# Optimization experiments

Hardware: AMD Instinct MI355X
Metric: run time of the kernel (lower is better)

## Reference

```python
import jax, jax.numpy as jnp
import numpy as np

D_G = 16384; B = 128; NNZ = 262144
CL1_F = 32; CL1_K = 6; FC1_F = 512; FC2_F = 512
NN_FC1 = 512; NN_FC2 = 256
CL4_F = 32; CL4_K = 4; FC1_G4 = 128; FC2_G4 = 64
OUT = 10; POOL1 = 8; POOL4 = 3; V4 = 10; EMB = 64
FC1FIN = CL1_F * (D_G // POOL1)        # 65536
G4OUT = CL4_F * (OUT // POOL4)         # 96
SUMFIN = FC1_F + NN_FC2 + FC2_G4 + 64  # 896


def _cheby(x, W, b, spmm, K):
    # x: [B, V, Fin]; Chebyshev recursion T_k(L) x with K-order feature stacking
    Bb, V, Fin = x.shape
    x0 = jnp.transpose(x, (1, 2, 0)).reshape(V, Fin * Bb)
    xs = [x0]
    if K > 1:
        x1 = spmm(x0)
        xs.append(x1)
        for _ in range(K - 2):
            x2 = 2.0 * spmm(x1) - x0
            xs.append(x2)
            x0, x1 = x1, x2
    X = jnp.stack(xs).reshape(K, V, Fin, Bb)
    X = jnp.transpose(X, (3, 1, 2, 0)).reshape(Bb * V, Fin * K)  # [B*V, Fin*K]
    return (X @ W.T + b).reshape(Bb, V, -1)


def _gmaxpool(x, p):
    # MaxPool1d(p) over node dim (floor truncation like torch)
    Bb, V, F = x.shape
    Vp = (V // p) * p
    return x[:, :Vp].reshape(Bb, V // p, p, F).max(axis=2)


def setup_inputs():
    key = jax.random.key(0)
    ks = jax.random.split(key, 32)
    def lin(i, fo, fi):
        return (jax.random.normal(ks[i], (fo, fi), jnp.float32) * 0.02,
                jnp.zeros((fo,), jnp.float32))
    cl1_W, cl1_b = lin(0, CL1_F, CL1_K)
    fc1_W, fc1_b = lin(1, FC1_F, FC1FIN)
    fc2_W, fc2_b = lin(2, FC2_F, FC1_F)
    fc3_W, fc3_b = lin(3, D_G, FC2_F)
    nn1_W, nn1_b = lin(4, NN_FC1, D_G)
    nn2_W, nn2_b = lin(5, NN_FC2, NN_FC1)
    cl4_W, cl4_b = lin(6, CL4_F, CL4_K * EMB)
    fcg1_W, fcg1_b = lin(7, FC1_G4, G4OUT)
    fcg2_W, fcg2_b = lin(8, FC2_G4, FC1_G4)
    nn14_W, nn14_b = lin(9, 256, V4 * EMB)
    nn24_W, nn24_b = lin(10, 64, 256)
    fcsum_W, fcsum_b = lin(11, OUT, SUMFIN)
    return {
        'x_in': jax.random.normal(ks[12], (B, D_G), jnp.float32),
        'x_embed': jax.random.normal(ks[13], (V4, EMB), jnp.float32),
        'dropout': 0,
        'L_rows': jnp.sort(jax.random.randint(ks[14], (NNZ,), 0, D_G)),
        'L_cols': jax.random.randint(ks[15], (NNZ,), 0, D_G),
        'L_vals': jax.random.normal(ks[16], (NNZ,), jnp.float32) * 0.1,
        'L_mg': jax.random.normal(ks[17], (V4, V4), jnp.float32) * 0.2,
        'cl1_W': cl1_W, 'cl1_b': cl1_b, 'fc1_W': fc1_W, 'fc1_b': fc1_b,
        'fc2_W': fc2_W, 'fc2_b': fc2_b, 'fc3_W': fc3_W, 'fc3_b': fc3_b,
        'nn1_W': nn1_W, 'nn1_b': nn1_b, 'nn2_W': nn2_W, 'nn2_b': nn2_b,
        'cl4_W': cl4_W, 'cl4_b': cl4_b, 'fcg1_W': fcg1_W, 'fcg1_b': fcg1_b,
        'fcg2_W': fcg2_W, 'fcg2_b': fcg2_b, 'nn14_W': nn14_W, 'nn14_b': nn14_b,
        'nn24_W': nn24_W, 'nn24_b': nn24_b, 'fcsum_W': fcsum_W, 'fcsum_b': fcsum_b,
    }


def reference(x_in, x_embed, dropout, L_rows, L_cols, L_vals, L_mg,
              cl1_W, cl1_b, fc1_W, fc1_b, fc2_W, fc2_b, fc3_W, fc3_b,
              nn1_W, nn1_b, nn2_W, nn2_b, cl4_W, cl4_b,
              fcg1_W, fcg1_b, fcg2_W, fcg2_b, nn14_W, nn14_b, nn24_W, nn24_b,
              fcsum_W, fcsum_b):
    Bb = x_in.shape[0]
    def spmm_L(m):  # COO SpMM: y[r] += v * m[c]
        return jax.ops.segment_sum(L_vals[:, None] * m[L_cols], L_rows,
                                   num_segments=D_G)
    # --- GCN 1 (gene graph) ---
    x = _cheby(x_in[:, :, None], cl1_W, cl1_b, spmm_L, CL1_K)
    x = jax.nn.relu(x)
    x = _gmaxpool(x, POOL1).reshape(Bb, FC1FIN)
    x_hidden_gae = jax.nn.relu(x @ fc1_W.T + fc1_b)
    # FC2_F != 0 branch; dropout p=0 is identity at this baseline
    x_decode_gae = jax.nn.relu(x_hidden_gae @ fc2_W.T + fc2_b)
    x_decode_gae = x_decode_gae @ fc3_W.T + fc3_b
    # --- NN 1 ---
    x_nn = jax.nn.relu(x_in @ nn1_W.T + nn1_b)
    x_nn = jax.nn.relu(x_nn @ nn2_W.T + nn2_b)
    # --- GCN 4 (small meta-graph, dense Laplacian) ---
    xe = jnp.broadcast_to(x_embed[None], (Bb, V4, EMB))
    xg = _cheby(xe, cl4_W, cl4_b, lambda m: L_mg @ m, CL4_K)
    xg = jax.nn.relu(xg)
    xg = _gmaxpool(xg, POOL4).reshape(Bb, G4OUT)
    xg = jax.nn.relu(xg @ fcg1_W.T + fcg1_b)
    xg = jax.nn.relu(xg @ fcg2_W.T + fcg2_b)
    # --- NN of GCN4 ---
    xn4 = xe.reshape(Bb, V4 * EMB)
    xn4 = jax.nn.relu(xn4 @ nn14_W.T + nn14_b)
    xn4 = jax.nn.relu(xn4 @ nn24_W.T + nn24_b)
    data_emb = jnp.concatenate([x_hidden_gae, x_nn, xg, xn4], axis=1)
    logp = jax.nn.log_softmax(data_emb @ fcsum_W.T + fcsum_b, axis=-1)
    return x_decode_gae, x_hidden_gae, logp
```

## Files before the change

kernel.cpp:

```cpp
#include <hip/hip_runtime.h>
#include <hip/hip_bf16.h>

#define DG 16384
#define NNZ 262144
#define BB 128

typedef __attribute__((ext_vector_type(8))) short bf16x8;
typedef __attribute__((ext_vector_type(8))) unsigned short us8;
typedef __attribute__((ext_vector_type(4))) float f32x4;
typedef __attribute__((ext_vector_type(4))) unsigned short us4;
typedef __attribute__((ext_vector_type(2))) float f32x2;

#define WS_ROWPTR 0
#define WS_XIN16  66048
#define WS_T      4260352
#define WS_XPOOL  54592000
#define WS_XB0    71369216
#define WS_XB1    75563520
#define WS_XNN1B  79757824
#define WS_DEC2   79888896
#define WS_XNN2   80019968
#define WS_HIDB   80151040
#define WS_N1     80282112
#define WS_TAIL   80283136
#define WS_PNN1   81000448
#define WS_PFC1   97777664

__device__ __forceinline__ unsigned short f2bf(float f) {
  __hip_bfloat16 h = __float2bfloat16(f);
  return __builtin_bit_cast(unsigned short, h);
}
__device__ __forceinline__ float bflo(unsigned u) {
  return __builtin_bit_cast(float, u << 16);
}
__device__ __forceinline__ float bfhi(unsigned u) {
  return __builtin_bit_cast(float, u & 0xffff0000u);
}
__device__ __forceinline__ f32x4 ntload4(const float* p) {
  return __builtin_nontemporal_load((const f32x4*)p);
}

__device__ void prep_dev(const float* __restrict__ x_in, const int* __restrict__ rows,
                         int* __restrict__ rowptr, unsigned short* __restrict__ xin16,
                         int bid) {
  int idx = bid * 256 + threadIdx.x;
  if (idx <= DG) {
    int lo = 0, hi = NNZ;
    while (lo < hi) { int mid = (lo + hi) >> 1; if (rows[mid] < idx) lo = mid + 1; else hi = mid; }
    rowptr[idx] = lo;
  }
  f32x4 v = ((const f32x4*)x_in)[idx];
  us4 o; o[0] = f2bf(v[0]); o[1] = f2bf(v[1]); o[2] = f2bf(v[2]); o[3] = f2bf(v[3]);
  ((us4*)xin16)[idx] = o;
}

__device__ void transpose_dev(const float* __restrict__ x_in, float* __restrict__ T0,
                              unsigned short* __restrict__ Xb0, int id) {
  __shared__ float tl[32][33];
  int bx = id & 511, by = id >> 9;
  int v0 = bx * 32, b0 = by * 32;
  int tx = threadIdx.x & 31, ty0 = threadIdx.x >> 5;
  #pragma unroll
  for (int j = 0; j < 4; ++j) {
    int ty = ty0 + j * 8;
    tl[ty][tx] = x_in[(size_t)(b0 + ty) * DG + v0 + tx];
  }
  __syncthreads();
  #pragma unroll
  for (int j = 0; j < 4; ++j) {
    int ty = ty0 + j * 8;
    float v = tl[tx][ty];
    size_t o = (size_t)(v0 + ty) * BB + b0 + tx;
    T0[o] = v;
    Xb0[o] = f2bf(v);
  }
}

__device__ void dot4_dev(const float* __restrict__ x, const float* __restrict__ W,
                         const float* __restrict__ bias, float* __restrict__ out,
                         int K, int id) {
  int w = threadIdx.x >> 6, lane = threadIdx.x & 63;
  int o = id * 4 + w;
  float a = 0.f;
  for (int i = lane; i < K; i += 64) a += x[i] * W[(size_t)o * K + i];
  #pragma unroll
  for (int s = 32; s > 0; s >>= 1) a += __shfl_down(a, s);
  if (lane == 0) out[o] = fmaxf(a + bias[o], 0.f);
}

__device__ void g4_dev(const float* __restrict__ xe_g, const float* __restrict__ Lmg_g,
                       const float* __restrict__ W4, const float* __restrict__ b4,
                       const float* __restrict__ Wg1, const float* __restrict__ bg1,
                       const float* __restrict__ Wg2, const float* __restrict__ bg2,
                       float* __restrict__ tail) {
  __shared__ float Lm[100], Tg[4][640], xc[320], xg96[96], h1[128];
  int t = threadIdx.x;
  for (int i = t; i < 640; i += 256) Tg[0][i] = xe_g[i];
  for (int i = t; i < 100; i += 256) Lm[i] = Lmg_g[i];
  __syncthreads();
  for (int i = t; i < 640; i += 256) {
    int v = i >> 6, f = i & 63; float s = 0.f;
    #pragma unroll
    for (int u = 0; u < 10; ++u) s += Lm[v * 10 + u] * Tg[0][u * 64 + f];
    Tg[1][i] = s;
  }
  __syncthreads();
  for (int kk = 2; kk < 4; ++kk) {
    for (int i = t; i < 640; i += 256) {
      int v = i >> 6, f = i & 63; float s = 0.f;
      #pragma unroll
      for (int u = 0; u < 10; ++u) s += Lm[v * 10 + u] * Tg[kk - 1][u * 64 + f];
      Tg[kk][i] = 2.f * s - Tg[kk - 2][i];
    }
    __syncthreads();
  }
  for (int i = t; i < 320; i += 256) {
    int v = i >> 5, fo = i & 31; float s = b4[fo];
    for (int fin = 0; fin < 64; ++fin)
      #pragma unroll
      for (int k = 0; k < 4; ++k) s += Tg[k][v * 64 + fin] * W4[fo * 256 + fin * 4 + k];
    xc[i] = fmaxf(s, 0.f);
  }
  __syncthreads();
  for (int i = t; i < 96; i += 256) {
    int g = i >> 5, fo = i & 31;
    xg96[i] = fmaxf(fmaxf(xc[(3 * g) * 32 + fo], xc[(3 * g + 1) * 32 + fo]),
                    xc[(3 * g + 2) * 32 + fo]);
  }
  __syncthreads();
  for (int o = t; o < 128; o += 256) {
    float s = bg1[o];
    for (int i2 = 0; i2 < 96; ++i2) s += xg96[i2] * Wg1[o * 96 + i2];
    h1[o] = fmaxf(s, 0.f);
  }
  __syncthreads();
  for (int o = t; o < 64; o += 256) {
    float s = bg2[o];
    for (int i2 = 0; i2 < 128; ++i2) s += h1[i2] * Wg2[o * 128 + i2];
    tail[o] = fmaxf(s, 0.f);
  }
}

__global__ __launch_bounds__(256) void setup_kernel(
    const float* __restrict__ x_in, const int* __restrict__ rows,
    int* __restrict__ rowptr, unsigned short* __restrict__ xin16,
    float* __restrict__ T0, unsigned short* __restrict__ Xb0,
    const float* __restrict__ x_embed,
    const float* __restrict__ nn14_W, const float* __restrict__ nn14_b,
    float* __restrict__ n1,
    const float* __restrict__ Lmg, const float* __restrict__ W4,
    const float* __restrict__ b4, const float* __restrict__ Wg1,
    const float* __restrict__ bg1, const float* __restrict__ Wg2,
    const float* __restrict__ bg2, float* __restrict__ tail) {
  int bid = blockIdx.x;
  if (bid < 1) g4_dev(x_embed, Lmg, W4, b4, Wg1, bg1, Wg2, bg2, tail);
  else if (bid < 65) dot4_dev(x_embed, nn14_W, nn14_b, n1, 640, bid - 1);
  else if (bid < 2113) prep_dev(x_in, rows, rowptr, xin16, bid - 65);
  else transpose_dev(x_in, T0, Xb0, bid - 2113);
}

__global__ __launch_bounds__(256) void spmm3(
    const int* __restrict__ rowptr, const int* __restrict__ cols,
    const float* __restrict__ vals, const unsigned* __restrict__ X2,
    const float* __restrict__ Tprev, float* __restrict__ Tout,
    unsigned* __restrict__ Xbout, float scale) {
  int r = blockIdx.x * 4 + (threadIdx.x >> 6);
  int lane = threadIdx.x & 63;
  int e0 = rowptr[r], e1 = rowptr[r + 1];
  float a00 = 0.f, a01 = 0.f, a10 = 0.f, a11 = 0.f;
  int e = e0;
  for (; e + 4 <= e1; e += 4) {
    int c0 = cols[e], c1 = cols[e + 1], c2 = cols[e + 2], c3 = cols[e + 3];
    float v0 = vals[e], v1 = vals[e + 1], v2 = vals[e + 2], v3 = vals[e + 3];
    unsigned x0 = X2[c0 * 64 + lane], x1 = X2[c1 * 64 + lane];
    unsigned x2 = X2[c2 * 64 + lane], x3 = X2[c3 * 64 + lane];
    a00 += v0 * bflo(x0); a10 += v0 * bfhi(x0);
    a01 += v1 * bflo(x1); a11 += v1 * bfhi(x1);
    a00 += v2 * bflo(x2); a10 += v2 * bfhi(x2);
    a01 += v3 * bflo(x3); a11 += v3 * bfhi(x3);
  }
  for (; e < e1; ++e) {
    float v = vals[e]; unsigned x = X2[cols[e] * 64 + lane];
    a00 += v * bflo(x); a10 += v * bfhi(x);
  }
  float s0 = scale * (a00 + a01), s1 = scale * (a10 + a11);
  size_t o = (size_t)r * BB + lane * 2;
  if (Tprev) { f32x2 p = *(const f32x2*)(Tprev + o); s0 -= p[0]; s1 -= p[1]; }
  *(f32x2*)(Tout + o) = (f32x2){s0, s1};
  Xbout[(size_t)r * 64 + lane] = (unsigned)f2bf(s0) | ((unsigned)f2bf(s1) << 16);
}

__device__ void combine_dev(const float* __restrict__ Tbase, const float* __restrict__ W,
                            const float* __restrict__ bias, unsigned short* __restrict__ xpool,
                            int vp) {
  __shared__ float tile[6][8][128];
  __shared__ float Wl[192];
  __shared__ float bl[32];
  for (int i = threadIdx.x; i < 192; i += 256) Wl[i] = W[i];
  if (threadIdx.x < 32) bl[threadIdx.x] = bias[threadIdx.x];
  for (int i = threadIdx.x; i < 6144; i += 256) {
    int k = i >> 10, rem = i & 1023, j = rem >> 7, b = rem & 127;
    tile[k][j][b] = Tbase[(size_t)k * 2097152 + (size_t)(vp * 8 + j) * BB + b];
  }
  __syncthreads();
  for (int p = threadIdx.x; p < 4096; p += 256) {
    int b = p >> 5, f = p & 31;
    float m = -1e30f;
    #pragma unroll
    for (int j = 0; j < 8; ++j) {
      float s = bl[f];
      #pragma unroll
      for (int k = 0; k < 6; ++k) s += tile[k][j][b] * Wl[f * 6 + k];
      m = fmaxf(m, s);
    }
    m = fmaxf(m, 0.f);
    xpool[(size_t)b * 65536 + vp * 32 + f] = f2bf(m);
  }
}

__global__ __launch_bounds__(256) void combine_nn24(
    const float* __restrict__ Tbase, const float* __restrict__ W,
    const float* __restrict__ bias, unsigned short* __restrict__ xpool,
    const float* __restrict__ n1, const float* __restrict__ nn24_W,
    const float* __restrict__ nn24_b, float* __restrict__ tail64) {
  int bid = blockIdx.x;
  if (bid < 2048) combine_dev(Tbase, W, bias, xpool, bid);
  else dot4_dev(n1, nn24_W, nn24_b, tail64, 256, bid - 2048);
}

template<int NT, int MT>
__device__ void gemm_core5(
    unsigned short* __restrict__ Alds,
    const unsigned short* __restrict__ A, const float* __restrict__ W,
    float* __restrict__ outP, unsigned short* __restrict__ outB,
    const float* __restrict__ bias, int K, int N, int Kchunk,
    int bx, int by, int row0, int relu, int partial) {
  const int LA = MT / 2;
  int t = threadIdx.x, w = t >> 6, lane = t & 63, lr = lane & 15, lg = lane >> 4;
  int n0 = bx * NT * 64;
  int kbeg = by * Kchunk;
  f32x4 acc[MT][NT];
  #pragma unroll
  for (int mt = 0; mt < MT; ++mt)
    #pragma unroll
    for (int nt = 0; nt < NT; ++nt) acc[mt][nt] = (f32x4){0.f, 0.f, 0.f, 0.f};
  const float* Wbase = W + (size_t)(n0 + w * NT * 16 + lr) * K + lg * 8;
  int stages = Kchunk >> 6;
  for (int s = 0; s < stages; ++s) {
    int k0 = kbeg + s * 64;
    f32x4 rw[NT][4];
    #pragma unroll
    for (int nt = 0; nt < NT; ++nt) {
      const float* wp = Wbase + (size_t)nt * 16 * K + k0;
      rw[nt][0] = ntload4(wp);      rw[nt][1] = ntload4(wp + 4);
      rw[nt][2] = ntload4(wp + 32); rw[nt][3] = ntload4(wp + 36);
    }
    __syncthreads();
    #pragma unroll
    for (int j = 0; j < LA; ++j) {
      int idx = j * 256 + t;
      int row = idx >> 3, kk = (idx & 7) * 8;
      us8 v = *(const us8*)(A + (size_t)(row0 + row) * K + k0 + kk);
      *(us8*)(Alds + row * 64 + (kk ^ ((row & 7) << 3))) = v;
    }
    __syncthreads();
    #pragma unroll
    for (int h = 0; h < 2; ++h) {
      int k32 = h * 32;
      bf16x8 bfr[NT];
      #pragma unroll
      for (int nt = 0; nt < NT; ++nt) {
        f32x4 w0 = rw[nt][h * 2], w1 = rw[nt][h * 2 + 1];
        bf16x8 bv;
        bv[0] = (short)f2bf(w0[0]); bv[1] = (short)f2bf(w0[1]);
        bv[2] = (short)f2bf(w0[2]); bv[3] = (short)f2bf(w0[3]);
        bv[4] = (short)f2bf(w1[0]); bv[5] = (short)f2bf(w1[1]);
        bv[6] = (short)f2bf(w1[2]); bv[7] = (short)f2bf(w1[3]);
        bfr[nt] = bv;
      }
      #pragma unroll
      for (int mt = 0; mt < MT; ++mt) {
        int arow = mt * 16 + lr;
        bf16x8 af = *(const bf16x8*)(Alds + arow * 64 + ((k32 + lg * 8) ^ ((arow & 7) << 3)));
        #pragma unroll
        for (int nt = 0; nt < NT; ++nt)
          acc[mt][nt] = __builtin_amdgcn_mfma_f32_16x16x32_bf16(af, bfr[nt], acc[mt][nt], 0, 0, 0);
      }
    }
  }
  if (partial) {
    float* P = outP + (size_t)by * 128 * (size_t)N;
    #pragma unroll
    for (int mt = 0; mt < MT; ++mt)
      #pragma unroll
      for (int nt = 0; nt < NT; ++nt) {
        int col = n0 + w * NT * 16 + nt * 16 + lr;
        #pragma unroll
        for (int r2 = 0; r2 < 4; ++r2) {
          int row = row0 + mt * 16 + lg * 4 + r2;
          P[(size_t)row * N + col] = acc[mt][nt][r2];
        }
      }
  } else {
    #pragma unroll
    for (int mt = 0; mt < MT; ++mt)
      #pragma unroll
      for (int nt = 0; nt < NT; ++nt) {
        int col = n0 + w * NT * 16 + nt * 16 + lr;
        float bc = bias[col];
        #pragma unroll
        for (int r2 = 0; r2 < 4; ++r2) {
          int row = row0 + mt * 16 + lg * 4 + r2;
          float v = acc[mt][nt][r2] + bc;
          if (relu) v = fmaxf(v, 0.f);
          if (outP) outP[(size_t)row * N + col] = v;
          if (outB) outB[(size_t)row * N + col] = f2bf(v);
        }
      }
  }
}

__global__ __launch_bounds__(256, 4) void gemm_partials(
    const unsigned short* __restrict__ xin16, const float* __restrict__ nn1_W,
    const unsigned short* __restrict__ xpool, const float* __restrict__ fc1_W,
    float* __restrict__ pnn1, float* __restrict__ pfc1) {
  __shared__ unsigned short Alds[128 * 64];
  int nb = blockIdx.x;
  if (nb < 128) {
    int xcd = nb & 7, q = nb >> 3, bx = q & 3, by = ((q >> 2) << 3) | xcd;
    gemm_core5<2, 8>(Alds, xin16, nn1_W, pnn1, nullptr, nullptr,
                     16384, 512, 512, bx, by, 0, 0, 1);
  } else {
    int b = nb - 128;
    int xcd = b & 7, q = b >> 3, bx = q & 3, by = ((q >> 2) << 3) | xcd;
    gemm_core5<2, 8>(Alds, xpool, fc1_W, pfc1, nullptr, nullptr,
                     65536, 512, 512, bx, by, 0, 0, 1);
  }
}

__global__ __launch_bounds__(256) void reduce_fused(
    const float* __restrict__ pfc1, const float* __restrict__ fc1_b,
    float* __restrict__ hidden, unsigned short* __restrict__ hidB,
    const float* __restrict__ pnn1, const float* __restrict__ nn1_b,
    unsigned short* __restrict__ xnn1b) {
  int b = blockIdx.x;
  if (b < 256) {
    int idx = b * 256 + threadIdx.x;
    float s = 0.f;
    for (int i = 0; i < 128; ++i) s += pfc1[(size_t)i * 65536 + idx];
    float v = fmaxf(s + fc1_b[idx & 511], 0.f);
    hidden[idx] = v;
    hidB[idx] = f2bf(v);
  } else {
    int idx = (b - 256) * 256 + threadIdx.x;
    float s = 0.f;
    for (int i = 0; i < 32; ++i) s += pnn1[(size_t)i * 65536 + idx];
    float v = fmaxf(s + nn1_b[idx & 511], 0.f);
    xnn1b[idx] = f2bf(v);
  }
}

__global__ __launch_bounds__(256, 4) void fc2nn2_kernel(
    const unsigned short* __restrict__ hidB, const float* __restrict__ fc2_W,
    const float* __restrict__ fc2_b, unsigned short* __restrict__ dec2,
    const unsigned short* __restrict__ xnn1b, const float* __restrict__ nn2_W,
    const float* __restrict__ nn2_b, float* __restrict__ xnn2) {
  __shared__ unsigned short Alds[128 * 64];
  int b = blockIdx.x;
  if (b < 8)
    gemm_core5<1, 8>(Alds, hidB, fc2_W, nullptr, dec2, fc2_b,
                     512, 512, 512, b, 0, 0, 1, 0);
  else
    gemm_core5<1, 8>(Alds, xnn1b, nn2_W, xnn2, nullptr, nn2_b,
                     512, 256, 512, b - 8, 0, 0, 1, 0);
}

__device__ void fcsum_dev(int id, const float* __restrict__ hidden,
                          const float* __restrict__ xnn2, const float* __restrict__ tail,
                          const float* __restrict__ Ws, const float* __restrict__ bs,
                          float* __restrict__ logp) {
  __shared__ float emb[4][896];
  int w = threadIdx.x >> 6, lane = threadIdx.x & 63;
  int b = id * 4 + w;
  for (int i = lane; i < 896; i += 64)
    emb[w][i] = (i < 512) ? hidden[b * 512 + i]
              : (i < 768) ? xnn2[b * 256 + (i - 512)]
                          : tail[i - 768];
  __syncthreads();
  float l[10];
  #pragma unroll
  for (int o = 0; o < 10; ++o) {
    float a = 0.f;
    for (int i = lane; i < 896; i += 64) a += emb[w][i] * Ws[o * 896 + i];
    #pragma unroll
    for (int s = 32; s > 0; s >>= 1) a += __shfl_down(a, s);
    l[o] = __shfl(a, 0) + bs[o];
  }
  float m = l[0];
  #pragma unroll
  for (int o = 1; o < 10; ++o) m = fmaxf(m, l[o]);
  float sum = 0.f;
  #pragma unroll
  for (int o = 0; o < 10; ++o) sum += expf(l[o] - m);
  float lse = m + logf(sum);
  #pragma unroll
  for (int o = 0; o < 10; ++o)
    if (lane == o) logp[b * 10 + o] = l[o] - lse;
}

__global__ __launch_bounds__(256, 4) void fc3_head(
    const unsigned short* __restrict__ dec2, const float* __restrict__ fc3_W,
    const float* __restrict__ fc3_b, float* __restrict__ out0,
    const float* __restrict__ hidden, const float* __restrict__ xnn2,
    const float* __restrict__ tail, const float* __restrict__ fcsum_W,
    const float* __restrict__ fcsum_b, float* __restrict__ logp) {
  __shared__ unsigned short Alds[64 * 64];
  int b = blockIdx.x;
  if (b < 512) {
    int bx = b >> 1, my = b & 1;
    gemm_core5<1, 4>(Alds, dec2, fc3_W, out0, nullptr, fc3_b,
                     512, 16384, 512, bx, 0, my * 64, 0, 0);
  } else {
    fcsum_dev(b - 512, hidden, xnn2, tail, fcsum_W, fcsum_b, logp);
  }
}

extern "C" void kernel_launch(void* const* d_in, const int* in_sizes, int n_in,
                              void* d_out, int out_size, void* d_ws, size_t ws_size,
                              hipStream_t stream) {
  const float* x_in    = (const float*)d_in[0];
  const float* x_embed = (const float*)d_in[1];
  const int*   L_rows  = (const int*)d_in[3];
  const int*   L_cols  = (const int*)d_in[4];
  const float* L_vals  = (const float*)d_in[5];
  const float* L_mg    = (const float*)d_in[6];
  const float* cl1_W = (const float*)d_in[7],  *cl1_b = (const float*)d_in[8];
  const float* fc1_W = (const float*)d_in[9],  *fc1_b = (const float*)d_in[10];
  const float* fc2_W = (const float*)d_in[11], *fc2_b = (const float*)d_in[12];
  const float* fc3_W = (const float*)d_in[13], *fc3_b = (const float*)d_in[14];
  const float* nn1_W = (const float*)d_in[15], *nn1_b = (const float*)d_in[16];
  const float* nn2_W = (const float*)d_in[17], *nn2_b = (const float*)d_in[18];
  const float* cl4_W = (const float*)d_in[19], *cl4_b = (const float*)d_in[20];
  const float* fcg1_W = (const float*)d_in[21], *fcg1_b = (const float*)d_in[22];
  const float* fcg2_W = (const float*)d_in[23], *fcg2_b = (const float*)d_in[24];
  const float* nn14_W = (const float*)d_in[25], *nn14_b = (const float*)d_in[26];
  const float* nn24_W = (const float*)d_in[27], *nn24_b = (const float*)d_in[28];
  const float* fcsum_W = (const float*)d_in[29], *fcsum_b = (const float*)d_in[30];

  char* ws = (char*)d_ws;
  int* rowptr = (int*)(ws + WS_ROWPTR);
  unsigned short* xin16 = (unsigned short*)(ws + WS_XIN16);
  float* T = (float*)(ws + WS_T);
  unsigned short* xpool = (unsigned short*)(ws + WS_XPOOL);
  unsigned short* Xb0 = (unsigned short*)(ws + WS_XB0);
  unsigned short* Xb1 = (unsigned short*)(ws + WS_XB1);
  unsigned short* xnn1b = (unsigned short*)(ws + WS_XNN1B);
  unsigned short* dec2 = (unsigned short*)(ws + WS_DEC2);
  float* xnn2 = (float*)(ws + WS_XNN2);
  unsigned short* hidB = (unsigned short*)(ws + WS_HIDB);
  float* n1 = (float*)(ws + WS_N1);
  float* tail = (float*)(ws + WS_TAIL);
  float* pnn1 = (float*)(ws + WS_PNN1);
  float* pfc1 = (float*)(ws + WS_PFC1);

  float* out0 = (float*)d_out;
  float* hidden = out0 + 2097152;
  float* logp = out0 + 2097152 + 65536;

  setup_kernel<<<4161, 256, 0, stream>>>(x_in, L_rows, rowptr, xin16, T, Xb0,
                                         x_embed, nn14_W, nn14_b, n1,
                                         L_mg, cl4_W, cl4_b, fcg1_W, fcg1_b,
                                         fcg2_W, fcg2_b, tail);

  spmm3<<<4096, 256, 0, stream>>>(rowptr, L_cols, L_vals, (const unsigned*)Xb0,
                                  nullptr,          T + 1 * 2097152, (unsigned*)Xb1, 1.f);
  spmm3<<<4096, 256, 0, stream>>>(rowptr, L_cols, L_vals, (const unsigned*)Xb1,
                                  T,                T + 2 * 2097152, (unsigned*)Xb0, 2.f);
  spmm3<<<4096, 256, 0, stream>>>(rowptr, L_cols, L_vals, (const unsigned*)Xb0,
                                  T + 1 * 2097152,  T + 3 * 2097152, (unsigned*)Xb1, 2.f);
  spmm3<<<4096, 256, 0, stream>>>(rowptr, L_cols, L_vals, (const unsigned*)Xb1,
                                  T + 2 * 2097152,  T + 4 * 2097152, (unsigned*)Xb0, 2.f);
  spmm3<<<4096, 256, 0, stream>>>(rowptr, L_cols, L_vals, (const unsigned*)Xb0,
                                  T + 3 * 2097152,  T + 5 * 2097152, (unsigned*)Xb1, 2.f);

  combine_nn24<<<2064, 256, 0, stream>>>(T, cl1_W, cl1_b, xpool,
                                         n1, nn24_W, nn24_b, tail + 64);

  gemm_partials<<<640, 256, 0, stream>>>(xin16, nn1_W, xpool, fc1_W, pnn1, pfc1);

  reduce_fused<<<512, 256, 0, stream>>>(pfc1, fc1_b, hidden, hidB,
                                        pnn1, nn1_b, xnn1b);

  fc2nn2_kernel<<<12, 256, 0, stream>>>(hidB, fc2_W, fc2_b, dec2,
                                        xnn1b, nn2_W, nn2_b, xnn2);

  fc3_head<<<544, 256, 0, stream>>>(dec2, fc3_W, fc3_b, out0,
                                    hidden, xnn2, tail, fcsum_W, fcsum_b, logp);
}
```

Baseline: 284.9 us.

## Stage converted weight tiles in LDS and use full 128-row tiles for fc2/nn2/fc3

Adds a GEMM core that loads each 64x64 fp32 weight tile once per stage, converts it to bf16 into swizzled shared memory, and has all waves read MFMA operands from LDS. The fc2/nn2 and fc3 kernels switch to this core, and fc3 now covers all 128 batch rows per block, so its grid halves and the fc3 weights are not re-read by two blocks. The cost is extra LDS traffic and a sync per stage, fewer blocks in flight for fc3, and the occupancy hint removed from launch bounds.

```diff
diff --git a/kernel.cpp b/kernel.cpp
--- a/kernel.cpp
+++ b/kernel.cpp
@@ -228,6 +228,93 @@
   else dot4_dev(n1, nn24_W, nn24_b, tail64, 256, bid - 2048);
 }
 
+template<int NT>
+__device__ void gemm_core(
+    unsigned short* __restrict__ Alds,
+    unsigned short* __restrict__ Wlds,
+    const unsigned short* __restrict__ A, const float* __restrict__ W,
+    float* __restrict__ outP, unsigned short* __restrict__ outB,
+    const float* __restrict__ bias, int K, int N, int Kchunk,
+    int bx, int by, int relu, int partial) {
+  int t = threadIdx.x, w = t >> 6, lane = t & 63, lr = lane & 15, lg = lane >> 4;
+  int n0 = bx * NT * 64;
+  int kbeg = by * Kchunk;
+  f32x4 acc[8][NT];
+  #pragma unroll
+  for (int mt = 0; mt < 8; ++mt)
+    #pragma unroll
+    for (int nt = 0; nt < NT; ++nt) acc[mt][nt] = (f32x4){0.f, 0.f, 0.f, 0.f};
+  int stages = Kchunk >> 6;
+  for (int s = 0; s < stages; ++s) {
+    int k0 = kbeg + s * 64;
+    __syncthreads();
+    #pragma unroll
+    for (int j = 0; j < 4; ++j) {
+      int idx = j * 256 + t;
+      int row = idx >> 3, kk = (idx & 7) * 8;
+      us8 v = *(const us8*)(A + (size_t)row * K + k0 + kk);
+      *(us8*)(Alds + row * 64 + (kk ^ ((row & 7) << 3))) = v;
+    }
+    #pragma unroll
+    for (int j = 0; j < NT * 4; ++j) {
+      int idx = j * 256 + t;
+      int wr = idx >> 4, kk = (idx & 15) * 4;
+      f32x4 v = *(const f32x4*)(W + (size_t)(n0 + wr) * K + k0 + kk);
+      us4 o; o[0] = f2bf(v[0]); o[1] = f2bf(v[1]); o[2] = f2bf(v[2]); o[3] = f2bf(v[3]);
+      *(us4*)(Wlds + wr * 64 + (kk ^ ((wr & 7) << 3))) = o;
+    }
+    __syncthreads();
+    #pragma unroll
+    for (int h = 0; h < 2; ++h) {
+      int k32 = h * 32;
+      bf16x8 bfr[NT];
+      #pragma unroll
+      for (int nt = 0; nt < NT; ++nt) {
+        int wrow = w * NT * 16 + nt * 16 + lr;
+        bfr[nt] = *(const bf16x8*)(Wlds + wrow * 64 + ((k32 + lg * 8) ^ ((wrow & 7) << 3)));
+      }
+      #pragma unroll
+      for (int mt = 0; mt < 8; ++mt) {
+        int arow = mt * 16 + lr;
+        bf16x8 af = *(const bf16x8*)(Alds + arow * 64 + ((k32 + lg * 8) ^ ((arow & 7) << 3)));
+        #pragma unroll
+        for (int nt = 0; nt < NT; ++nt)
+          acc[mt][nt] = __builtin_amdgcn_mfma_f32_16x16x32_bf16(af, bfr[nt], acc[mt][nt], 0, 0, 0);
+      }
+    }
+  }
+  if (partial) {
+    float* P = outP + (size_t)by * 128 * (size_t)N;
+    #pragma unroll
+    for (int mt = 0; mt < 8; ++mt)
+      #pragma unroll
+      for (int nt = 0; nt < NT; ++nt) {
+        int col = n0 + w * NT * 16 + nt * 16 + lr;
+        #pragma unroll
+        for (int r2 = 0; r2 < 4; ++r2) {
+          int row = mt * 16 + lg * 4 + r2;
+          P[(size_t)row * N + col] = acc[mt][nt][r2];
+        }
+      }
+  } else {
+    #pragma unroll
+    for (int mt = 0; mt < 8; ++mt)
+      #pragma unroll
+      for (int nt = 0; nt < NT; ++nt) {
+        int col = n0 + w * NT * 16 + nt * 16 + lr;
+        float bc = bias[col];
+        #pragma unroll
+        for (int r2 = 0; r2 < 4; ++r2) {
+          int row = mt * 16 + lg * 4 + r2;
+          float v = acc[mt][nt][r2] + bc;
+          if (relu) v = fmaxf(v, 0.f);
+          if (outP) outP[(size_t)row * N + col] = v;
+          if (outB) outB[(size_t)row * N + col] = f2bf(v);
+        }
+      }
+  }
+}
+
 template<int NT, int MT>
 __device__ void gemm_core5(
     unsigned short* __restrict__ Alds,
@@ -360,19 +447,20 @@
   }
 }
 
-__global__ __launch_bounds__(256, 4) void fc2nn2_kernel(
+__global__ __launch_bounds__(256) void fc2nn2_kernel(
     const unsigned short* __restrict__ hidB, const float* __restrict__ fc2_W,
     const float* __restrict__ fc2_b, unsigned short* __restrict__ dec2,
     const unsigned short* __restrict__ xnn1b, const float* __restrict__ nn2_W,
     const float* __restrict__ nn2_b, float* __restrict__ xnn2) {
   __shared__ unsigned short Alds[128 * 64];
+  __shared__ unsigned short Wlds[64 * 64];
   int b = blockIdx.x;
   if (b < 8)
-    gemm_core5<1, 8>(Alds, hidB, fc2_W, nullptr, dec2, fc2_b,
-                     512, 512, 512, b, 0, 0, 1, 0);
+    gemm_core<1>(Alds, Wlds, hidB, fc2_W, nullptr, dec2, fc2_b,
+                 512, 512, 512, b, 0, 1, 0);
   else
-    gemm_core5<1, 8>(Alds, xnn1b, nn2_W, xnn2, nullptr, nn2_b,
-                     512, 256, 512, b - 8, 0, 0, 1, 0);
+    gemm_core<1>(Alds, Wlds, xnn1b, nn2_W, xnn2, nullptr, nn2_b,
+                 512, 256, 512, b - 8, 0, 1, 0);
 }
 
 __device__ void fcsum_dev(int id, const float* __restrict__ hidden,
@@ -408,21 +496,20 @@
     if (lane == o) logp[b * 10 + o] = l[o] - lse;
 }
 
-__global__ __launch_bounds__(256, 4) void fc3_head(
+__global__ __launch_bounds__(256) void fc3_head(
     const unsigned short* __restrict__ dec2, const float* __restrict__ fc3_W,
     const float* __restrict__ fc3_b, float* __restrict__ out0,
     const float* __restrict__ hidden, const float* __restrict__ xnn2,
     const float* __restrict__ tail, const float* __restrict__ fcsum_W,
     const float* __restrict__ fcsum_b, float* __restrict__ logp) {
-  __shared__ unsigned short Alds[64 * 64];
+  __shared__ unsigned short Alds[128 * 64];
+  __shared__ unsigned short Wlds[64 * 64];
   int b = blockIdx.x;
-  if (b < 512) {
-    int bx = b >> 1, my = b & 1;
-    gemm_core5<1, 4>(Alds, dec2, fc3_W, out0, nullptr, fc3_b,
-                     512, 16384, 512, bx, 0, my * 64, 0, 0);
-  } else {
-    fcsum_dev(b - 512, hidden, xnn2, tail, fcsum_W, fcsum_b, logp);
-  }
+  if (b < 256)
+    gemm_core<1>(Alds, Wlds, dec2, fc3_W, out0, nullptr, fc3_b,
+                 512, 16384, 512, b, 0, 0, 0);
+  else
+    fcsum_dev(b - 256, hidden, xnn2, tail, fcsum_W, fcsum_b, logp);
 }
 
 extern "C" void kernel_launch(void* const* d_in, const int* in_sizes, int n_in,
@@ -494,6 +581,6 @@
   fc2nn2_kernel<<<12, 256, 0, stream>>>(hidB, fc2_W, fc2_b, dec2,
                                         xnn1b, nn2_W, nn2_b, xnn2);
 
-  fc3_head<<<544, 256, 0, stream>>>(dec2, fc3_W, fc3_b, out0,
+  fc3_head<<<288, 256, 0, stream>>>(dec2, fc3_W, fc3_b, out0,
                                     hidden, xnn2, tail, fcsum_W, fcsum_b, logp);
 }
```

Result: faster. 267.3 us (-6.2%).
